# Performance work log

Measured on AMD Instinct MI355X. Metric: run time of the kernel, lower is better.

## Reference

```python
import jax, jax.numpy as jnp
import numpy as np

MARLIN_TILE = 16   # rows of W packed per int32 row of B
GROUP = 128        # quantization group size along in_features


def _dequantize(B, s):
    """Unpack int4 nibbles from int32-packed B and apply group scales.

    B: int32 [in//16, out*2] -- each int32 holds 8 4-bit values.
    s: float  [in//GROUP, out] -- per-group, per-output-channel scales.
    Returns W: float [in, out].
    Reference packing: B reshaped to [in//16, out, 2] int32s; the 2x8 nibbles
    (little-endian within each int32) form the 16 input rows of the tile.
    """
    n_tiles, twice_out = B.shape
    out_f = twice_out // 2
    in_f = n_tiles * MARLIN_TILE
    shifts = jnp.arange(8, dtype=jnp.int32) * 4                 # nibble shifts
    packed = B.reshape(n_tiles, out_f, 2)                        # [T, O, 2]
    nibbles = (packed[..., None] >> shifts) & 0xF                # [T, O, 2, 8]
    q = nibbles.reshape(n_tiles, out_f, MARLIN_TILE)             # [T, O, 16]
    q = jnp.transpose(q, (0, 2, 1)).reshape(in_f, out_f)         # [in, out]
    qf = (q.astype(s.dtype) - 8.0)                               # symmetric int4
    scales = jnp.repeat(s, GROUP, axis=0)                        # [in, out]
    return qf * scales


def setup_inputs() -> dict:
    key = jax.random.key(0)
    k1, k2, k3, k4 = jax.random.split(key, 4)
    M, IN_F, OUT_F = 4096, 4096, 12288
    A = jax.random.normal(k1, (M, IN_F), dtype=jnp.float32)
    B = jax.random.randint(k2, (IN_F // MARLIN_TILE, OUT_F * 2), 0,
                           2147483647, dtype=jnp.int32)
    s = jax.random.uniform(k3, (IN_F // GROUP, OUT_F), dtype=jnp.float32) * 0.01
    bias = jax.random.normal(k4, (OUT_F,), dtype=jnp.float32) * 0.01
    return {"A": A, "B": B, "s": s, "bias": bias}


def reference(A, B, s, bias):
    W = _dequantize(B, s)                      # [in, out]
    C = jnp.matmul(A, W) + bias                # [M, out]
    return C
```

## Files before the change

kernel.cpp:

```cpp
#include <hip/hip_runtime.h>
#include <hip/hip_bf16.h>

typedef __bf16 bf16x8 __attribute__((ext_vector_type(8)));
typedef float floatx4 __attribute__((ext_vector_type(4)));

#define AS1 __attribute__((address_space(1)))
#define AS3 __attribute__((address_space(3)))

__global__ __launch_bounds__(256) void cvt_a_kernel(const float* __restrict__ A,
                                                    __hip_bfloat16* __restrict__ Ab,
                                                    int n8) {
    int i = blockIdx.x * 256 + threadIdx.x;
    if (i >= n8) return;
    size_t base = (size_t)i * 8;
    float4 a0 = *(const float4*)(A + base);
    float4 a1 = *(const float4*)(A + base + 4);
    union { __hip_bfloat16 h[8]; float4 f; } u;
    u.h[0] = __float2bfloat16(a0.x);
    u.h[1] = __float2bfloat16(a0.y);
    u.h[2] = __float2bfloat16(a0.z);
    u.h[3] = __float2bfloat16(a0.w);
    u.h[4] = __float2bfloat16(a1.x);
    u.h[5] = __float2bfloat16(a1.y);
    u.h[6] = __float2bfloat16(a1.z);
    u.h[7] = __float2bfloat16(a1.w);
    *(float4*)(Ab + base) = u.f;
}

__global__ __launch_bounds__(256) void dequant_kernel(const int* __restrict__ Bp,
                                                      const float* __restrict__ s,
                                                      __hip_bfloat16* __restrict__ Wt,
                                                      int N, int T) {
    const int tid = threadIdx.x;
    const int tl = tid & 15;
    const int nl = tid >> 4;
    const int t = blockIdx.x * 16 + tl;
    const int n = blockIdx.y * 16 + nl;
    const int2 p = *(const int2*)(Bp + (size_t)t * (2 * N) + 2 * n);
    const unsigned lo = (unsigned)p.x;
    const unsigned hi = (unsigned)p.y;
    const float sc = s[(size_t)(t >> 3) * N + n];
    union { __hip_bfloat16 h[16]; float4 f[2]; } u;
#pragma unroll
    for (int r = 0; r < 8; ++r) {
        u.h[r]     = __float2bfloat16(((float)((lo >> (4 * r)) & 0xFu) - 8.0f) * sc);
        u.h[r + 8] = __float2bfloat16(((float)((hi >> (4 * r)) & 0xFu) - 8.0f) * sc);
    }
    float4* dst = (float4*)(Wt + (size_t)n * ((size_t)T * 16) + (size_t)t * 16);
    dst[0] = u.f[0];
    dst[1] = u.f[1];
}

__global__ __launch_bounds__(256) void gemm_bt_kernel(const __hip_bfloat16* __restrict__ A,
                                                      const __hip_bfloat16* __restrict__ Bt,
                                                      const float* __restrict__ bias,
                                                      float* __restrict__ C,
                                                      int M, int N, int K) {
    __shared__ __hip_bfloat16 As[128 * 64];
    __shared__ __hip_bfloat16 Bs[128 * 64];

    const int tid = threadIdx.x;
    const int wave = tid >> 6;
    const int lane = tid & 63;
    const int m0 = blockIdx.y * 128;
    const int n0 = blockIdx.x * 128;
    const int wm = wave >> 1;
    const int wn = wave & 1;

    floatx4 acc[4][4];
#pragma unroll
    for (int i = 0; i < 4; ++i)
#pragma unroll
        for (int j = 0; j < 4; ++j) acc[i][j] = (floatx4){0.f, 0.f, 0.f, 0.f};

    const int ldrow = wave * 8 + (lane >> 3);
    const int swz = lane >> 3;
    const int ldcol = (((lane & 7) ^ swz)) * 8;
    const __hip_bfloat16* Aldg = A + (size_t)(m0 + ldrow) * K + ldcol;
    const __hip_bfloat16* Bldg = Bt + (size_t)(n0 + ldrow) * K + ldcol;
    __hip_bfloat16* AsBase = &As[(wave * 8) * 64];
    __hip_bfloat16* BsBase = &Bs[(wave * 8) * 64];

    for (int k0 = 0; k0 < K; k0 += 64) {
#pragma unroll
        for (int i = 0; i < 4; ++i) {
            __builtin_amdgcn_global_load_lds((AS1 void*)(Aldg + (size_t)(i * 32) * K + k0),
                                             (AS3 void*)(AsBase + i * 32 * 64), 16, 0, 0);
            __builtin_amdgcn_global_load_lds((AS1 void*)(Bldg + (size_t)(i * 32) * K + k0),
                                             (AS3 void*)(BsBase + i * 32 * 64), 16, 0, 0);
        }
        __syncthreads();

#pragma unroll
        for (int ks = 0; ks < 2; ++ks) {
            const int koff = ((ks * 4 + (lane >> 4)) ^ (lane & 7)) * 8;
            bf16x8 af[4], bfr[4];
#pragma unroll
            for (int i = 0; i < 4; ++i)
                af[i] = *(const bf16x8*)&As[(wm * 64 + i * 16 + (lane & 15)) * 64 + koff];
#pragma unroll
            for (int j = 0; j < 4; ++j)
                bfr[j] = *(const bf16x8*)&Bs[(wn * 64 + j * 16 + (lane & 15)) * 64 + koff];
#pragma unroll
            for (int i = 0; i < 4; ++i)
#pragma unroll
                for (int j = 0; j < 4; ++j)
                    acc[i][j] = __builtin_amdgcn_mfma_f32_16x16x32_bf16(af[i], bfr[j],
                                                                        acc[i][j], 0, 0, 0);
        }
        __syncthreads();
    }

    const int cl = lane & 15;
    const int rq = (lane >> 4) * 4;
#pragma unroll
    for (int j = 0; j < 4; ++j) {
        const int n = n0 + wn * 64 + j * 16 + cl;
        const float bv = bias[n];
#pragma unroll
        for (int i = 0; i < 4; ++i) {
            const int mbase = m0 + wm * 64 + i * 16 + rq;
#pragma unroll
            for (int r = 0; r < 4; ++r)
                C[(size_t)(mbase + r) * N + n] = acc[i][j][r] + bv;
        }
    }
}

extern "C" void kernel_launch(void* const* d_in, const int* in_sizes, int n_in,
                              void* d_out, int out_size, void* d_ws, size_t ws_size,
                              hipStream_t stream) {
    const float* A = (const float*)d_in[0];
    const int* Bp = (const int*)d_in[1];
    const float* s = (const float*)d_in[2];
    const float* bias = (const float*)d_in[3];
    float* C = (float*)d_out;

    const int N = in_sizes[3];
    const long Bsz = (long)in_sizes[1];
    const int K = (int)(Bsz / (2L * N)) * 16;
    const int M = (int)((long)in_sizes[0] / K);
    const int T = K / 16;

    __hip_bfloat16* Ab = (__hip_bfloat16*)d_ws;
    __hip_bfloat16* Wt = (__hip_bfloat16*)((char*)d_ws + (size_t)M * K * 2);

    const int n8 = (M * K) / 8;
    cvt_a_kernel<<<(n8 + 255) / 256, 256, 0, stream>>>(A, Ab, n8);
    dequant_kernel<<<dim3(T / 16, N / 16), 256, 0, stream>>>(Bp, s, Wt, N, T);
    gemm_bt_kernel<<<dim3(N / 128, M / 128), 256, 0, stream>>>(Ab, Wt, bias, C, M, N, K);
}
```

Baseline: 761.1 us.

## Stage dequant output through LDS, swizzle GEMM block order, nontemporal C stores

The dequant kernel now processes 64 output channels by 16 K-tiles per block and stages the results in shared memory. This lets each output row of Wt be written as contiguous 512-byte runs instead of scattered 32-byte pieces. The GEMM remaps block indices so that groups of 8 N-column blocks sweep all M rows, aiming for better L2 reuse of B tiles. Output C is written with nontemporal stores so it does not pollute the cache. Together these add index math and an LDS round trip in dequant.

Result: faster. 731.0 us (-4.0%).

```diff
diff --git a/kernel.cpp b/kernel.cpp
--- a/kernel.cpp
+++ b/kernel.cpp
@@ -31,24 +31,48 @@
                                                       const float* __restrict__ s,
                                                       __hip_bfloat16* __restrict__ Wt,
                                                       int N, int T) {
+    __shared__ __hip_bfloat16 tile[64][264];
     const int tid = threadIdx.x;
-    const int tl = tid & 15;
-    const int nl = tid >> 4;
-    const int t = blockIdx.x * 16 + tl;
-    const int n = blockIdx.y * 16 + nl;
-    const int2 p = *(const int2*)(Bp + (size_t)t * (2 * N) + 2 * n);
-    const unsigned lo = (unsigned)p.x;
-    const unsigned hi = (unsigned)p.y;
-    const float sc = s[(size_t)(t >> 3) * N + n];
-    union { __hip_bfloat16 h[16]; float4 f[2]; } u;
+    const int t0 = blockIdx.x * 16;
+    const int n0 = blockIdx.y * 64;
+    const int K = T * 16;
+
+    {
+        const int nl = tid & 63;
+        const int tg = tid >> 6;
 #pragma unroll
-    for (int r = 0; r < 8; ++r) {
-        u.h[r]     = __float2bfloat16(((float)((lo >> (4 * r)) & 0xFu) - 8.0f) * sc);
-        u.h[r + 8] = __float2bfloat16(((float)((hi >> (4 * r)) & 0xFu) - 8.0f) * sc);
+        for (int tt = 0; tt < 4; ++tt) {
+            const int tl = tg * 4 + tt;
+            const int t = t0 + tl;
+            const int n = n0 + nl;
+            const int2 p = *(const int2*)(Bp + (size_t)t * (2 * N) + 2 * n);
+            const unsigned lo = (unsigned)p.x;
+            const unsigned hi = (unsigned)p.y;
+            const float sc = s[(size_t)(t >> 3) * N + n];
+            union { __hip_bfloat16 h[16]; float4 f[2]; } u;
+#pragma unroll
+            for (int r = 0; r < 8; ++r) {
+                u.h[r]     = __float2bfloat16(((float)((lo >> (4 * r)) & 0xFu) - 8.0f) * sc);
+                u.h[r + 8] = __float2bfloat16(((float)((hi >> (4 * r)) & 0xFu) - 8.0f) * sc);
+            }
+            *(float4*)&tile[nl][tl * 16]     = u.f[0];
+            *(float4*)&tile[nl][tl * 16 + 8] = u.f[1];
+        }
     }
-    float4* dst = (float4*)(Wt + (size_t)n * ((size_t)T * 16) + (size_t)t * 16);
-    dst[0] = u.f[0];
-    dst[1] = u.f[1];
+    __syncthreads();
+    {
+        const int tl = tid & 15;
+        const int nq = tid >> 4;
+#pragma unroll
+        for (int p = 0; p < 4; ++p) {
+            const int n = p * 16 + nq;
+            float4 v0 = *(const float4*)&tile[n][tl * 16];
+            float4 v1 = *(const float4*)&tile[n][tl * 16 + 8];
+            float4* dst = (float4*)(Wt + (size_t)(n0 + n) * K + (size_t)(t0 + tl) * 16);
+            dst[0] = v0;
+            dst[1] = v1;
+        }
+    }
 }
 
 __global__ __launch_bounds__(256) void gemm_bt_kernel(const __hip_bfloat16* __restrict__ A,
@@ -59,11 +83,24 @@
     __shared__ __hip_bfloat16 As[128 * 64];
     __shared__ __hip_bfloat16 Bs[128 * 64];
 
+    int bx, by;
+    {
+        const int flat = blockIdx.y * gridDim.x + blockIdx.x;
+        const int gy = gridDim.y;
+        const int per = 8 * gy;
+        const int g = flat / per;
+        const int r = flat - g * per;
+        const int xi = r / gy;
+        bx = g * 8 + xi;
+        by = r - xi * gy;
+        if (bx >= (int)gridDim.x) { bx = blockIdx.x; by = blockIdx.y; }
+    }
+
     const int tid = threadIdx.x;
     const int wave = tid >> 6;
     const int lane = tid & 63;
-    const int m0 = blockIdx.y * 128;
-    const int n0 = blockIdx.x * 128;
+    const int m0 = by * 128;
+    const int n0 = bx * 128;
     const int wm = wave >> 1;
     const int wn = wave & 1;
 
@@ -121,8 +158,10 @@
         for (int i = 0; i < 4; ++i) {
             const int mbase = m0 + wm * 64 + i * 16 + rq;
 #pragma unroll
-            for (int r = 0; r < 4; ++r)
-                C[(size_t)(mbase + r) * N + n] = acc[i][j][r] + bv;
+            for (int r = 0; r < 4; ++r) {
+                float v = acc[i][j][r] + bv;
+                __builtin_nontemporal_store(v, &C[(size_t)(mbase + r) * N + n]);
+            }
         }
     }
 }
@@ -147,6 +186,6 @@
 
     const int n8 = (M * K) / 8;
     cvt_a_kernel<<<(n8 + 255) / 256, 256, 0, stream>>>(A, Ab, n8);
-    dequant_kernel<<<dim3(T / 16, N / 16), 256, 0, stream>>>(Bp, s, Wt, N, T);
+    dequant_kernel<<<dim3(T / 16, N / 64), 256, 0, stream>>>(Bp, s, Wt, N, T);
     gemm_bt_kernel<<<dim3(N / 128, M / 128), 256, 0, stream>>>(Ab, Wt, bias, C, M, N, K);
 }
```
